# Performance work log

Measured on AMD Instinct MI355X. Metric: run time of the kernel, lower is better.

## Reference

```python
import jax, jax.numpy as jnp
import numpy as np

D_MODEL = 1024
B, T_Q, T_KV = 4, 2048, 2048


def _linear_params(key, d_in, d_out):
    kw, kb = jax.random.split(key)
    W = jax.random.normal(kw, (d_out, d_in), dtype=jnp.float32) * 0.02
    b = jax.random.normal(kb, (d_out,), dtype=jnp.float32) * 0.02
    return W, b


def setup_inputs() -> dict:
    key = jax.random.key(0)
    ks = jax.random.split(key, 7)
    latent_space = jax.random.normal(ks[0], (B, T_Q, D_MODEL), dtype=jnp.float32)
    input_space = jax.random.normal(ks[1], (B, T_KV, D_MODEL), dtype=jnp.float32)
    Wl, bl = _linear_params(ks[2], D_MODEL, D_MODEL)
    Wu, bu = _linear_params(ks[3], D_MODEL, D_MODEL)
    WA, bA = _linear_params(ks[4], D_MODEL, D_MODEL)  # A_proj: d -> J (J = d)
    WV, bV = _linear_params(ks[5], D_MODEL, D_MODEL)  # V_proj: J -> d
    Wo, bo = _linear_params(ks[6], D_MODEL, D_MODEL)
    return {
        "latent_space": latent_space, "input_space": input_space,
        "Wl": Wl, "bl": bl, "Wu": Wu, "bu": bu,
        "WA": WA, "bA": bA, "WV": WV, "bV": bV,
        "Wo": Wo, "bo": bo,
    }


def reference(latent_space, input_space, Wl, bl, Wu, bu, WA, bA, WV, bV, Wo, bo):
    # emb_0 = l_proj(latent)            [B, T_q, d]
    emb0 = jnp.einsum('bqd,ed->bqe', latent_space, Wl) + bl
    # l = softmax(u_proj(emb_0), -1)^T  [B, d, T_q]
    l = jax.nn.softmax(jnp.einsum('bqd,ed->bqe', emb0, Wu) + bu, axis=-1)
    l = jnp.swapaxes(l, -2, -1)
    # D = A_proj(input)                 [B, T_kv, J]
    Dm = jnp.einsum('bkd,jd->bkj', input_space, WA) + bA
    # A = softmax(V_proj(D), dim=-2)    softmax over T_kv
    A = jax.nn.softmax(jnp.einsum('bkj,dj->bkd', Dm, WV) + bV, axis=-2)
    # w = A @ l                         [B, T_kv, T_q]
    w = jnp.einsum('bkd,bdq->bkq', A, l)
    # o = w @ o_proj(latent)            [B, T_kv, d]
    ov = jnp.einsum('bqd,ed->bqe', latent_space, Wo) + bo
    o = jnp.einsum('bkq,bqd->bkd', w, ov)
    return o
```

## Files before the change

kernel.cpp:

```cpp
#include <hip/hip_runtime.h>
#include <hip/hip_bf16.h>
#include <stdint.h>

typedef __attribute__((ext_vector_type(8))) short bf16x8;
typedef __attribute__((ext_vector_type(4))) float f32x4;
typedef __attribute__((ext_vector_type(4))) unsigned short u16x4;

#define B_  4
#define T_  2048
#define D_  1024

__device__ __forceinline__ float bf2f(ushort u) {
  union { unsigned int i; float f; } v; v.i = ((unsigned int)u) << 16; return v.f;
}
__device__ __forceinline__ ushort f2bf(float f) {
  return (ushort)(__bfloat16_as_ushort(__float2bfloat16(f)));
}
__device__ __forceinline__ void async16(const void* g, void* l) {
  __builtin_amdgcn_global_load_lds(
      (const __attribute__((address_space(1))) void*)g,
      (__attribute__((address_space(3))) void*)l, 16, 0, 0);
}

__global__ __launch_bounds__(256)
void prep(const float* __restrict__ lat, const float* __restrict__ inp,
          const float* __restrict__ Wl, const float* __restrict__ bl,
          const float* __restrict__ Wu, const float* __restrict__ bu,
          const float* __restrict__ WA, const float* __restrict__ bA,
          const float* __restrict__ WV, const float* __restrict__ bV,
          const float* __restrict__ Wo, const float* __restrict__ bo,
          ushort* __restrict__ xBf, ushort* __restrict__ xBf2,
          ushort* __restrict__ w1, ushort* __restrict__ w2,
          ushort* __restrict__ wCatWo, float* __restrict__ bc, float* __restrict__ bc2)
{
  __shared__ alignas(16) ushort t[64 * 65];
  const long NW = (long)D_ * D_;
  const int bx = blockIdx.x;
  const int tid = threadIdx.x;
  if (bx < 16384) {
    const float* in = bx < 8192 ? lat : inp;
    ushort* out = bx < 8192 ? xBf : xBf2;
    const long i = (long)(bx & 8191) * 256 + tid;
    const float4 v = *(const float4*)(in + i * 4);
    u16x4 o;
    o[0] = f2bf(v.x); o[1] = f2bf(v.y); o[2] = f2bf(v.z); o[3] = f2bf(v.w);
    *(u16x4*)(out + i * 4) = o;
  } else if (bx < 19456) {
    const int seg = (bx - 16384) >> 10;
    const float* in  = seg == 0 ? Wu : (seg == 1 ? WV : Wo);
    ushort* out = seg == 0 ? w1 : (seg == 1 ? w1 + NW : wCatWo);
    const long i = (long)((bx - 16384) & 1023) * 256 + tid;
    const float4 v = *(const float4*)(in + i * 4);
    u16x4 o;
    o[0] = f2bf(v.x); o[1] = f2bf(v.y); o[2] = f2bf(v.z); o[3] = f2bf(v.w);
    *(u16x4*)(out + i * 4) = o;
  } else if (bx < 19968) {
    const int z = (bx - 19456) >> 8;
    const int w = (bx - 19456) & 255;
    const float* in = z ? WA : Wl;
    ushort* out = z ? w2 + NW : w2;
    const int c0 = (w & 15) * 64, r0 = (w >> 4) * 64;
    const int tx = tid & 15, ty = tid >> 4;
#pragma unroll
    for (int i = 0; i < 4; ++i) {
      const int r = ty + i * 16;
      const float4 v = *(const float4*)(in + (long)(r0 + r) * D_ + c0 + tx * 4);
      t[(tx * 4 + 0) * 65 + r] = f2bf(v.x);
      t[(tx * 4 + 1) * 65 + r] = f2bf(v.y);
      t[(tx * 4 + 2) * 65 + r] = f2bf(v.z);
      t[(tx * 4 + 3) * 65 + r] = f2bf(v.w);
    }
    __syncthreads();
#pragma unroll
    for (int i = 0; i < 4; ++i) {
      const int c = ty + i * 16;
      u16x4 v;
#pragma unroll
      for (int j = 0; j < 4; ++j) v[j] = t[c * 65 + tx * 4 + j];
      *(u16x4*)(out + (long)(c0 + c) * D_ + r0 + tx * 4) = v;
    }
  } else {
    const int z = (bx - 19968) >> 8;
    const int w = (bx - 19968) & 255;
    const float* W    = z ? WV : Wu;
    const float* bin  = z ? bA : bl;
    const float* badd = z ? bV : bu;
    float* out        = z ? bc2 : bc;
    const int wv = tid >> 6, lane = tid & 63;
    const int e = w * 4 + wv;
    const float* row = W + (long)e * D_;
    float s = 0.f;
#pragma unroll
    for (int i = 0; i < 16; ++i) s += row[lane + i * 64] * bin[lane + i * 64];
#pragma unroll
    for (int off = 32; off; off >>= 1) s += __shfl_xor(s, off);
    if (lane == 0) out[e] = s + badd[e];
  }
}

#define PH_SYNC_IN()                                               \
  __builtin_amdgcn_s_barrier();                                    \
  asm volatile("s_waitcnt lgkmcnt(0)" ::: "memory");               \
  __builtin_amdgcn_sched_barrier(0);                               \
  __builtin_amdgcn_s_setprio(1)
#define PH_SYNC_OUT()                                              \
  __builtin_amdgcn_s_setprio(0);                                   \
  __builtin_amdgcn_s_barrier()


__global__ __launch_bounds__(512, 2)
void gemm256(const ushort* __restrict__ A, const ushort* __restrict__ Bm,
             const float* __restrict__ bias1, const float* __restrict__ bias2,
             ushort* __restrict__ C1, ushort* __restrict__ C2,
             int ldA, int ldB)
{
  __shared__ alignas(16) ushort AbS[2 * 16384];
  __shared__ alignas(16) ushort BbS[3 * 16384];

  const int gx = gridDim.x;
  const int nwg = gx * gridDim.y;
  int fid = blockIdx.y * gx + blockIdx.x;
  fid = (fid & 7) * (nwg >> 3) + (fid >> 3);
  const int bx = fid % gx;
  const int by = fid / gx;
  const int tileM = by * 256, tileN = bx * 256;

  const int tid  = threadIdx.x;
  const int wid  = tid >> 6;
  const int lane = tid & 63;
  const int wm   = wid >> 2;
  const int wn   = wid & 3;

  const int srow8 = tid >> 3;
  const int scol8 = ((tid & 7) ^ (srow8 & 7)) << 3;
  const ushort* gAs = A  + (long)(tileM + srow8) * ldA + scol8;
  const ushort* gBs = Bm + (long)(tileN + srow8) * ldB + scol8;
  const int sdst = tid << 3;

#define STA(b, i, t) async16(gAs + (long)((i) * 64) * ldA + (t) * 64, \
                             AbS + (b) * 16384 + (i) * 4096 + sdst)
#define STB(b, i, t) async16(gBs + (long)((i) * 64) * ldB + (t) * 64, \
                             BbS + (b) * 16384 + (i) * 4096 + sdst)

  const int frow = lane & 15;
  const int kg   = lane >> 4;
  const int ck0 = ((kg       ^ (frow & 7)) << 3);
  const int ck1 = (((4 + kg) ^ (frow & 7)) << 3);
  int aoffr[8], boffr[4];
#pragma unroll
  for (int mi = 0; mi < 8; ++mi) aoffr[mi] = (wm * 128 + mi * 16 + frow) * 64;
#pragma unroll
  for (int n = 0; n < 4; ++n)    boffr[n]  = (wn * 64 + n * 16 + frow) * 64;

  f32x4 acc[8][4];
#pragma unroll
  for (int i = 0; i < 8; ++i)
#pragma unroll
    for (int j = 0; j < 4; ++j) acc[i][j] = (f32x4){0.f, 0.f, 0.f, 0.f};

#pragma unroll
  for (int i = 0; i < 4; ++i) STA(0, i, 0);
#pragma unroll
  for (int i = 0; i < 4; ++i) STB(0, i, 0);
#pragma unroll
  for (int i = 0; i < 4; ++i) STA(1, i, 1);
#pragma unroll
  for (int i = 0; i < 4; ++i) STB(1, i, 1);
  asm volatile("s_waitcnt vmcnt(8)" ::: "memory");
  __builtin_amdgcn_s_barrier();

#pragma unroll 1
  for (int t = 0; t < 16; ++t) {
    const int buf = t & 1;
    const int bB  = t - (t / 3) * 3;
    const int nA  = (t + 1) & 1;
    const int nB  = (t + 2) - ((t + 2) / 3) * 3;
    const ushort* Ac = AbS + buf * 16384;
    const ushort* Bc = BbS + bB * 16384;
    bf16x8 fa[4], fb[4], ga[4];

#pragma unroll
    for (int n = 0; n < 4; ++n) fb[n] = *(const bf16x8*)(Bc + boffr[n] + ck0);
#pragma unroll
    for (int m = 0; m < 4; ++m) fa[m] = *(const bf16x8*)(Ac + aoffr[m] + ck0);
    if (t >= 1 && t <= 14) { STA(nA, 0, t + 1); STA(nA, 1, t + 1); }
    PH_SYNC_IN();
#pragma unroll
    for (int m = 0; m < 4; ++m)
#pragma unroll
      for (int n = 0; n < 4; ++n)
        acc[m][n] = __builtin_amdgcn_mfma_f32_16x16x32_bf16(fa[m], fb[n], acc[m][n], 0, 0, 0);
    PH_SYNC_OUT();

#pragma unroll
    for (int m = 0; m < 4; ++m) ga[m] = *(const bf16x8*)(Ac + aoffr[4 + m] + ck0);
    if (t >= 1 && t <= 14) { STA(nA, 2, t + 1); STA(nA, 3, t + 1); }
    if (t <= 13)           { STB(nB, 0, t + 2); STB(nB, 1, t + 2); }
    PH_SYNC_IN();
#pragma unroll
    for (int m = 0; m < 4; ++m)
#pragma unroll
      for (int n = 0; n < 4; ++n)
        acc[4 + m][n] = __builtin_amdgcn_mfma_f32_16x16x32_bf16(ga[m], fb[n], acc[4 + m][n], 0, 0, 0);
    PH_SYNC_OUT();

#pragma unroll
    for (int n = 0; n < 4; ++n) fb[n] = *(const bf16x8*)(Bc + boffr[n] + ck1);
#pragma unroll
    for (int m = 0; m < 4; ++m) fa[m] = *(const bf16x8*)(Ac + aoffr[m] + ck1);
    if (t <= 13) { STB(nB, 2, t + 2); STB(nB, 3, t + 2); }
    PH_SYNC_IN();
#pragma unroll
    for (int m = 0; m < 4; ++m)
#pragma unroll
      for (int n = 0; n < 4; ++n)
        acc[m][n] = __builtin_amdgcn_mfma_f32_16x16x32_bf16(fa[m], fb[n], acc[m][n], 0, 0, 0);
    PH_SYNC_OUT();

#pragma unroll
    for (int m = 0; m < 4; ++m) ga[m] = *(const bf16x8*)(Ac + aoffr[4 + m] + ck1);
    if (t <= 13)      { asm volatile("s_waitcnt vmcnt(4)" ::: "memory"); }
    else if (t == 14) { asm volatile("s_waitcnt vmcnt(0)" ::: "memory"); }
    PH_SYNC_IN();
#pragma unroll
    for (int m = 0; m < 4; ++m)
#pragma unroll
      for (int n = 0; n < 4; ++n)
        acc[4 + m][n] = __builtin_amdgcn_mfma_f32_16x16x32_bf16(ga[m], fb[n], acc[4 + m][n], 0, 0, 0);
    PH_SYNC_OUT();
  }
#undef STA
#undef STB

  const bool second = tileN >= 1024;
  ushort* Cp = second ? C2 : C1;
  const float* bb = second ? bias2 : bias1;
  const int cb = tileN - (second ? 1024 : 0) + wn * 64 + (lane & 15);
  const int rb = tileM + wm * 128 + ((lane >> 4) << 2);
#pragma unroll
  for (int mi = 0; mi < 8; ++mi) {
    const int mrow = rb + mi * 16;
#pragma unroll
    for (int ni = 0; ni < 4; ++ni) {
      const int col = cb + ni * 16;
      const float bv = bb[col];
#pragma unroll
      for (int r = 0; r < 4; ++r)
        Cp[(long)(mrow + r) * 1024 + col] = f2bf(acc[mi][ni][r] + bv);
    }
  }
}

template<int MODE>
__global__ __launch_bounds__(512, 2)
void gemm128(const ushort* __restrict__ A, const ushort* __restrict__ Bm,
             const float* __restrict__ bias1, void* __restrict__ C1,
             int ldA, int ldB, long sAz, long sBz, long sCz)
{
  __shared__ alignas(16) ushort AbS[3 * 16384];
  __shared__ alignas(16) ushort BbS[3 * 8192];

  const int gx = gridDim.x, gy = gridDim.y;
  const int nwg = gx * gy * gridDim.z;
  int fid = (blockIdx.z * gy + blockIdx.y) * gx + blockIdx.x;
  fid = (fid & 7) * (nwg >> 3) + (fid >> 3);
  const int bx = fid % gx;
  const int by = (fid / gx) % gy;
  const int bz = fid / (gx * gy);
  const int tileM = by * 256, tileN = bx * 128;

  const ushort* Ap = A;
  const ushort* Bp = Bm;
  if constexpr (MODE == 2) {
    Ap += (long)(bz >> 1) * sAz + (long)(bz & 1) * 1024;
    Bp += (long)(bz >> 1) * sBz + (long)(bz & 1) * 1024;
  } else {
    Ap += (long)bz * sAz;
    Bp += (long)bz * sBz;
  }

  const int tid  = threadIdx.x;
  const int wid  = tid >> 6;
  const int lane = tid & 63;
  const int wm   = wid >> 1;
  const int wn   = wid & 1;

  const int srow8 = tid >> 3;
  const int scol8 = ((tid & 7) ^ (srow8 & 7)) << 3;
  const ushort* gAs = Ap + (long)(tileM + srow8) * ldA + scol8;
  const ushort* gBs = Bp + (long)(tileN + srow8) * ldB + scol8;
  const int sdst = tid << 3;

#define STA(b, i, t) async16(gAs + (long)((i) * 64) * ldA + (t) * 64, \
                             AbS + (b) * 16384 + (i) * 4096 + sdst)
#define STB(b, i, t) async16(gBs + (long)((i) * 64) * ldB + (t) * 64, \
                             BbS + (b) * 8192 + (i) * 4096 + sdst)

  const int frow = lane & 15;
  const int kg   = lane >> 4;
  const int ck0 = ((kg       ^ (frow & 7)) << 3);
  const int ck1 = (((4 + kg) ^ (frow & 7)) << 3);
  int aoffr[4], boffr[4];
#pragma unroll
  for (int mi = 0; mi < 4; ++mi) aoffr[mi] = (wm * 64 + mi * 16 + frow) * 64;
#pragma unroll
  for (int n = 0; n < 4; ++n)    boffr[n]  = (wn * 64 + n * 16 + frow) * 64;

  f32x4 acc[4][4];
#pragma unroll
  for (int i = 0; i < 4; ++i)
#pragma unroll
    for (int j = 0; j < 4; ++j) acc[i][j] = (f32x4){0.f, 0.f, 0.f, 0.f};

#pragma unroll
  for (int i = 0; i < 4; ++i) STA(0, i, 0);
  STB(0, 0, 0); STB(0, 1, 0);
#pragma unroll
  for (int i = 0; i < 4; ++i) STA(1, i, 1);
  STB(1, 0, 1); STB(1, 1, 1);
  asm volatile("s_waitcnt vmcnt(6)" ::: "memory");
  __builtin_amdgcn_s_barrier();

#pragma unroll 1
  for (int t = 0; t < 16; ++t) {
    const int bufT = t - (t / 3) * 3;
    const int nb   = (t + 2) - ((t + 2) / 3) * 3;
    const ushort* Ac = AbS + bufT * 16384;
    const ushort* Bc = BbS + bufT * 8192;
    bf16x8 fa[4], fb[4];

#pragma unroll
    for (int n = 0; n < 4; ++n) fb[n] = *(const bf16x8*)(Bc + boffr[n] + ck0);
#pragma unroll
    for (int m = 0; m < 4; ++m) fa[m] = *(const bf16x8*)(Ac + aoffr[m] + ck0);
    if (t <= 13) { STA(nb, 0, t + 2); STA(nb, 1, t + 2); STA(nb, 2, t + 2); STA(nb, 3, t + 2); }
    PH_SYNC_IN();
#pragma unroll
    for (int m = 0; m < 4; ++m)
#pragma unroll
      for (int n = 0; n < 4; ++n)
        acc[m][n] = __builtin_amdgcn_mfma_f32_16x16x32_bf16(fa[m], fb[n], acc[m][n], 0, 0, 0);
    PH_SYNC_OUT();

#pragma unroll
    for (int n = 0; n < 4; ++n) fb[n] = *(const bf16x8*)(Bc + boffr[n] + ck1);
#pragma unroll
    for (int m = 0; m < 4; ++m) fa[m] = *(const bf16x8*)(Ac + aoffr[m] + ck1);
    if (t <= 13) { STB(nb, 0, t + 2); STB(nb, 1, t + 2); }
    if (t <= 13)      { asm volatile("s_waitcnt vmcnt(6)" ::: "memory"); }
    else if (t == 14) { asm volatile("s_waitcnt vmcnt(0)" ::: "memory"); }
    PH_SYNC_IN();
#pragma unroll
    for (int m = 0; m < 4; ++m)
#pragma unroll
      for (int n = 0; n < 4; ++n)
        acc[m][n] = __builtin_amdgcn_mfma_f32_16x16x32_bf16(fa[m], fb[n], acc[m][n], 0, 0, 0);
    PH_SYNC_OUT();
  }
#undef STA
#undef STB

  const int cb = tileN + wn * 64 + (lane & 15);
  const int rb = tileM + wm * 64 + ((lane >> 4) << 2);

  if constexpr (MODE == 0) {
    ushort* Cp = (ushort*)C1 + (long)bz * sCz;
#pragma unroll
    for (int ni = 0; ni < 4; ++ni) {
      const int col = cb + ni * 16;
#pragma unroll
      for (int mi = 0; mi < 4; ++mi)
#pragma unroll
        for (int r = 0; r < 4; ++r)
          Cp[(long)(rb + mi * 16 + r) * 1024 + col] = f2bf(acc[mi][ni][r]);
    }
  } else if constexpr (MODE == 1) {
    ushort* Cp = (ushort*)C1;
#pragma unroll
    for (int ni = 0; ni < 4; ++ni) {
      const int col = cb + ni * 16;
      const float bv = bias1[col];
#pragma unroll
      for (int mi = 0; mi < 4; ++mi)
#pragma unroll
        for (int r = 0; r < 4; ++r)
          Cp[(long)(rb + mi * 16 + r) * 1024 + col] = f2bf(__expf(acc[mi][ni][r] + bv));
    }
  } else if constexpr (MODE == 2) {
    ushort* Cp = (ushort*)C1 + ((long)(bz & 1) * B_ + (bz >> 1)) * ((long)D_ * D_);
#pragma unroll
    for (int ni = 0; ni < 4; ++ni) {
      const int col = cb + ni * 16;
#pragma unroll
      for (int mi = 0; mi < 4; ++mi)
#pragma unroll
        for (int r = 0; r < 4; ++r)
          Cp[(long)(rb + mi * 16 + r) * 1024 + col] = f2bf(acc[mi][ni][r]);
    }
  } else {
    float* Cp = (float*)C1 + (long)bz * sCz;
#pragma unroll
    for (int ni = 0; ni < 4; ++ni) {
      const int col = cb + ni * 16;
#pragma unroll
      for (int mi = 0; mi < 4; ++mi)
#pragma unroll
        for (int r = 0; r < 4; ++r)
          Cp[(long)(rb + mi * 16 + r) * 1024 + col] = acc[mi][ni][r];
    }
  }
}

__global__ __launch_bounds__(256)
void reduce2_scale(const ushort* __restrict__ P, const float* __restrict__ cinv,
                   ushort* __restrict__ MT)
{
  const long stride = (long)B_ * D_ * D_;
  const long base = ((long)blockIdx.x * 256 + threadIdx.x) * 8;
  const int b = (int)(base >> 20);
  const int e0 = (int)(base & (D_ - 1));
  bf16x8 p0 = *(const bf16x8*)(P + base);
  bf16x8 p1 = *(const bf16x8*)(P + stride + base);
  const float4 c0 = *(const float4*)(cinv + (long)b * D_ + e0);
  const float4 c1 = *(const float4*)(cinv + (long)b * D_ + e0 + 4);
  const float cc[8] = {c0.x, c0.y, c0.z, c0.w, c1.x, c1.y, c1.z, c1.w};
  bf16x8 o;
#pragma unroll
  for (int j = 0; j < 8; ++j)
    o[j] = (short)f2bf((bf2f((ushort)p0[j]) + bf2f((ushort)p1[j])) * cc[j]);
  *(bf16x8*)(MT + base) = o;
}

__global__ __launch_bounds__(256)
void softmax_row(ushort* __restrict__ S)
{
  const long base = (long)blockIdx.x * D_;
  const int tid = threadIdx.x;
  float e[4], s = 0.f;
#pragma unroll
  for (int i = 0; i < 4; ++i) { e[i] = __expf(bf2f(S[base + i * 256 + tid])); s += e[i]; }
#pragma unroll
  for (int off = 32; off; off >>= 1) s += __shfl_xor(s, off);
  __shared__ float reds[4];
  if ((tid & 63) == 0) reds[tid >> 6] = s;
  __syncthreads();
  s = reds[0] + reds[1] + reds[2] + reds[3];
  const float inv = 1.f / s;
#pragma unroll
  for (int i = 0; i < 4; ++i)
    S[base + i * 256 + tid] = f2bf(e[i] * inv);
}

__global__ __launch_bounds__(256)
void transpose2(const ushort* __restrict__ l, ushort* __restrict__ lT,
                const ushort* __restrict__ ov, ushort* __restrict__ ovT)
{
  __shared__ alignas(16) ushort t[64 * 65];
  const int z = blockIdx.z;
  const int b = z & (B_ - 1);
  const ushort* in = (z < B_ ? l : ov) + (long)b * T_ * D_;
  ushort* out      = (z < B_ ? lT : ovT) + (long)b * (long)D_ * T_;
  const int c0 = blockIdx.x * 64, r0 = blockIdx.y * 64;
  const int tx = threadIdx.x & 15, ty = threadIdx.x >> 4;
#pragma unroll
  for (int i = 0; i < 4; ++i) {
    const int r = ty + i * 16;
    u16x4 v = *(const u16x4*)(in + (long)(r0 + r) * D_ + c0 + tx * 4);
#pragma unroll
    for (int c = 0; c < 4; ++c) t[(tx * 4 + c) * 65 + r] = v[c];
  }
  __syncthreads();
#pragma unroll
  for (int i = 0; i < 4; ++i) {
    const int c = ty + i * 16;
    u16x4 v;
#pragma unroll
    for (int j = 0; j < 4; ++j) v[j] = t[c * 65 + tx * 4 + j];
    *(u16x4*)(out + (long)(c0 + c) * T_ + r0 + tx * 4) = v;
  }
}

__global__ __launch_bounds__(256)
void colsum_part(const ushort* __restrict__ E, float* __restrict__ psum)
{
  const int d = blockIdx.x * 256 + threadIdx.x;
  const int c = blockIdx.y;
  const int b = blockIdx.z;
  const ushort* p = E + ((long)b * T_ + (long)c * 128) * D_ + d;
  float s = 0.f;
#pragma unroll 4
  for (int r = 0; r < 128; ++r) s += bf2f(p[(long)r * D_]);
  psum[((long)b * 16 + c) * D_ + d] = s;
}

__global__ __launch_bounds__(256)
void colsum_comb(const float* __restrict__ psum, float* __restrict__ cinv)
{
  const int d = blockIdx.x * 256 + threadIdx.x;
  const int b = blockIdx.y;
  float s = 0.f;
#pragma unroll
  for (int c = 0; c < 16; ++c) s += psum[((long)b * 16 + c) * D_ + d];
  cinv[(long)b * D_ + d] = 1.f / s;
}

extern "C" void kernel_launch(void* const* d_in, const int* in_sizes, int n_in,
                              void* d_out, int out_size, void* d_ws, size_t ws_size,
                              hipStream_t stream)
{
  (void)in_sizes; (void)n_in; (void)out_size; (void)ws_size;
  const float* lat = (const float*)d_in[0];
  const float* inp = (const float*)d_in[1];
  const float* Wl  = (const float*)d_in[2];
  const float* bl  = (const float*)d_in[3];
  const float* Wu  = (const float*)d_in[4];
  const float* bu  = (const float*)d_in[5];
  const float* WA  = (const float*)d_in[6];
  const float* bA  = (const float*)d_in[7];
  const float* WV  = (const float*)d_in[8];
  const float* bV  = (const float*)d_in[9];
  const float* Wo  = (const float*)d_in[10];
  const float* bo  = (const float*)d_in[11];

  char* w = (char*)d_ws;
  auto carve = [&](size_t bytes) { char* p = w; w += (bytes + 255) & ~(size_t)255; return p; };
  const long NT = (long)B_ * T_ * D_;
  const long NW = (long)D_ * D_;
  ushort* xBf   = (ushort*)carve(NT * 2);
  ushort* xBf2  = (ushort*)carve(NT * 2);
  ushort* bufA  = (ushort*)carve(NT * 2);
  ushort* bufB  = (ushort*)carve(NT * 2);
  ushort* scr   = (ushort*)carve(NT * 2);
  ushort* MT    = (ushort*)carve((long)B_ * NW * 2);
  ushort* wCat  = (ushort*)carve(3 * NW * 2);
  float*  bc    = (float*)carve(D_ * 4);
  float*  bc2   = (float*)carve(D_ * 4);
  float*  psum  = (float*)carve(64 * 1024 * 4);
  float*  cinv  = (float*)carve(8 * 1024 * 4);
  ushort* w1 = scr;
  ushort* w2 = scr + 2 * NW;
  ushort* ovT = scr;
  ushort* part = bufB;

  const dim3 blk(256, 1, 1);
  const dim3 blk5(512, 1, 1);

  prep<<<dim3(20480), blk, 0, stream>>>(lat, inp, Wl, bl, Wu, bu, WA, bA, WV, bV, Wo, bo,
                                        xBf, xBf2, w1, w2, wCat + NW, bc, bc2);
  gemm128<0><<<dim3(8, 4, 2), blk5, 0, stream>>>(
      w1, w2, nullptr, wCat, D_, D_, NW, NW, 2 * NW);
  gemm256<<<dim3(8, 32, 1), blk5, 0, stream>>>(
      xBf, wCat, bc, bo, bufB, bufA, D_, D_);
  softmax_row<<<dim3(B_ * T_), blk, 0, stream>>>(bufB);
  transpose2<<<dim3(16, 32, 2 * B_), blk, 0, stream>>>(bufB, xBf, bufA, ovT);
  gemm128<2><<<dim3(8, 4, 8), blk5, 0, stream>>>(
      ovT, xBf, nullptr, part, T_, T_, (long)D_ * T_, (long)D_ * T_, 0);
  gemm128<1><<<dim3(8, 32, 1), blk5, 0, stream>>>(
      xBf2, wCat + 2 * NW, bc2, bufA, D_, D_, 0, 0, 0);
  colsum_part<<<dim3(4, 16, B_), blk, 0, stream>>>(bufA, psum);
  colsum_comb<<<dim3(4, B_, 1), blk, 0, stream>>>(psum, cinv);
  reduce2_scale<<<dim3(2048), blk, 0, stream>>>(part, cinv, MT);
  gemm128<3><<<dim3(8, 8, 4), blk5, 0, stream>>>(
      bufA, MT, nullptr, d_out, D_, D_,
      (long)T_ * D_, NW, (long)T_ * D_);
}
```

Before: 309.6 us.

## Split-K weight product, fuse column sums into GEMM epilogue, fold softmax into transpose

The weight-product GEMM is now split-K four ways across 256 blocks, with a separate reduce kernel, to raise parallelism over the previous 64-block launch. The column-sum for the softmax over T_kv is folded into the exp GEMM epilogue as wave shuffles plus atomicAdd, with psum zeroed in prep, which removes the two colsum kernels. Row softmax is split into a read-only row-sum kernel, and the normalisation moves into the transpose, saving one write and one read of the full activation. Costs are atomic contention, an extra exp per element, split-K partials rounded to bf16 before summation, and a nondeterministic summation order.

New measurement: 292.0 us. 1.06x faster.

```diff
diff --git a/kernel.cpp b/kernel.cpp
--- a/kernel.cpp
+++ b/kernel.cpp
@@ -31,7 +31,8 @@
           const float* __restrict__ Wo, const float* __restrict__ bo,
           ushort* __restrict__ xBf, ushort* __restrict__ xBf2,
           ushort* __restrict__ w1, ushort* __restrict__ w2,
-          ushort* __restrict__ wCatWo, float* __restrict__ bc, float* __restrict__ bc2)
+          ushort* __restrict__ wCatWo, float* __restrict__ bc, float* __restrict__ bc2,
+          float* __restrict__ psum)
 {
   __shared__ alignas(16) ushort t[64 * 65];
   const long NW = (long)D_ * D_;
@@ -79,7 +80,7 @@
       for (int j = 0; j < 4; ++j) v[j] = t[c * 65 + tx * 4 + j];
       *(u16x4*)(out + (long)(c0 + c) * D_ + r0 + tx * 4) = v;
     }
-  } else {
+  } else if (bx < 20480) {
     const int z = (bx - 19968) >> 8;
     const int w = (bx - 19968) & 255;
     const float* W    = z ? WV : Wu;
@@ -95,6 +96,8 @@
 #pragma unroll
     for (int off = 32; off; off >>= 1) s += __shfl_xor(s, off);
     if (lane == 0) out[e] = s + badd[e];
+  } else {
+    psum[(bx - 20480) * 256 + tid] = 0.f;
   }
 }
 
@@ -106,7 +109,6 @@
 #define PH_SYNC_OUT()                                              \
   __builtin_amdgcn_s_setprio(0);                                   \
   __builtin_amdgcn_s_barrier()
-
 
 __global__ __launch_bounds__(512, 2)
 void gemm256(const ushort* __restrict__ A, const ushort* __restrict__ Bm,
@@ -251,11 +253,12 @@
   }
 }
 
-template<int MODE>
+template<int MODE, int NKT = 16>
 __global__ __launch_bounds__(512, 2)
 void gemm128(const ushort* __restrict__ A, const ushort* __restrict__ Bm,
              const float* __restrict__ bias1, void* __restrict__ C1,
-             int ldA, int ldB, long sAz, long sBz, long sCz)
+             int ldA, int ldB, long sAz, long sBz, long sCz,
+             float* __restrict__ psumG)
 {
   __shared__ alignas(16) ushort AbS[3 * 16384];
   __shared__ alignas(16) ushort BbS[3 * 8192];
@@ -274,6 +277,9 @@
   if constexpr (MODE == 2) {
     Ap += (long)(bz >> 1) * sAz + (long)(bz & 1) * 1024;
     Bp += (long)(bz >> 1) * sBz + (long)(bz & 1) * 1024;
+  } else if constexpr (MODE == 4) {
+    Ap += (long)(bz >> 2) * sAz + (long)(bz & 3) * 256;
+    Bp += (long)(bz >> 2) * sBz + (long)(bz & 3) * 256;
   } else {
     Ap += (long)bz * sAz;
     Bp += (long)bz * sBz;
@@ -322,7 +328,7 @@
   __builtin_amdgcn_s_barrier();
 
 #pragma unroll 1
-  for (int t = 0; t < 16; ++t) {
+  for (int t = 0; t < NKT; ++t) {
     const int bufT = t - (t / 3) * 3;
     const int nb   = (t + 2) - ((t + 2) / 3) * 3;
     const ushort* Ac = AbS + bufT * 16384;
@@ -333,7 +339,7 @@
     for (int n = 0; n < 4; ++n) fb[n] = *(const bf16x8*)(Bc + boffr[n] + ck0);
 #pragma unroll
     for (int m = 0; m < 4; ++m) fa[m] = *(const bf16x8*)(Ac + aoffr[m] + ck0);
-    if (t <= 13) { STA(nb, 0, t + 2); STA(nb, 1, t + 2); STA(nb, 2, t + 2); STA(nb, 3, t + 2); }
+    if (t <= NKT - 3) { STA(nb, 0, t + 2); STA(nb, 1, t + 2); STA(nb, 2, t + 2); STA(nb, 3, t + 2); }
     PH_SYNC_IN();
 #pragma unroll
     for (int m = 0; m < 4; ++m)
@@ -346,9 +352,9 @@
     for (int n = 0; n < 4; ++n) fb[n] = *(const bf16x8*)(Bc + boffr[n] + ck1);
 #pragma unroll
     for (int m = 0; m < 4; ++m) fa[m] = *(const bf16x8*)(Ac + aoffr[m] + ck1);
-    if (t <= 13) { STB(nb, 0, t + 2); STB(nb, 1, t + 2); }
-    if (t <= 13)      { asm volatile("s_waitcnt vmcnt(6)" ::: "memory"); }
-    else if (t == 14) { asm volatile("s_waitcnt vmcnt(0)" ::: "memory"); }
+    if (t <= NKT - 3) { STB(nb, 0, t + 2); STB(nb, 1, t + 2); }
+    if (t <= NKT - 3)      { asm volatile("s_waitcnt vmcnt(6)" ::: "memory"); }
+    else if (t == NKT - 2) { asm volatile("s_waitcnt vmcnt(0)" ::: "memory"); }
     PH_SYNC_IN();
 #pragma unroll
     for (int m = 0; m < 4; ++m)
@@ -363,28 +369,25 @@
   const int cb = tileN + wn * 64 + (lane & 15);
   const int rb = tileM + wm * 64 + ((lane >> 4) << 2);
 
-  if constexpr (MODE == 0) {
-    ushort* Cp = (ushort*)C1 + (long)bz * sCz;
-#pragma unroll
-    for (int ni = 0; ni < 4; ++ni) {
-      const int col = cb + ni * 16;
-#pragma unroll
-      for (int mi = 0; mi < 4; ++mi)
-#pragma unroll
-        for (int r = 0; r < 4; ++r)
-          Cp[(long)(rb + mi * 16 + r) * 1024 + col] = f2bf(acc[mi][ni][r]);
-    }
-  } else if constexpr (MODE == 1) {
+  if constexpr (MODE == 1) {
     ushort* Cp = (ushort*)C1;
+    const int bE = tileM >> 11;
 #pragma unroll
     for (int ni = 0; ni < 4; ++ni) {
       const int col = cb + ni * 16;
       const float bv = bias1[col];
+      float cs = 0.f;
 #pragma unroll
       for (int mi = 0; mi < 4; ++mi)
 #pragma unroll
-        for (int r = 0; r < 4; ++r)
-          Cp[(long)(rb + mi * 16 + r) * 1024 + col] = f2bf(__expf(acc[mi][ni][r] + bv));
+        for (int r = 0; r < 4; ++r) {
+          const ushort ev = f2bf(__expf(acc[mi][ni][r] + bv));
+          Cp[(long)(rb + mi * 16 + r) * 1024 + col] = ev;
+          cs += bf2f(ev);
+        }
+      cs += __shfl_xor(cs, 16);
+      cs += __shfl_xor(cs, 32);
+      if ((lane >> 4) == 0) atomicAdd(psumG + (long)bE * D_ + col, cs);
     }
   } else if constexpr (MODE == 2) {
     ushort* Cp = (ushort*)C1 + ((long)(bz & 1) * B_ + (bz >> 1)) * ((long)D_ * D_);
@@ -397,6 +400,18 @@
         for (int r = 0; r < 4; ++r)
           Cp[(long)(rb + mi * 16 + r) * 1024 + col] = f2bf(acc[mi][ni][r]);
     }
+  } else if constexpr (MODE == 4) {
+    const int comp = bz >> 2, sp = bz & 3;
+    ushort* Cp = (ushort*)C1 + ((long)sp * 2 + comp) * ((long)D_ * D_);
+#pragma unroll
+    for (int ni = 0; ni < 4; ++ni) {
+      const int col = cb + ni * 16;
+#pragma unroll
+      for (int mi = 0; mi < 4; ++mi)
+#pragma unroll
+        for (int r = 0; r < 4; ++r)
+          Cp[(long)(rb + mi * 16 + r) * 1024 + col] = f2bf(acc[mi][ni][r]);
+    }
   } else {
     float* Cp = (float*)C1 + (long)bz * sCz;
 #pragma unroll
@@ -412,7 +427,80 @@
 }
 
 __global__ __launch_bounds__(256)
-void reduce2_scale(const ushort* __restrict__ P, const float* __restrict__ cinv,
+void reduce4(const ushort* __restrict__ P, ushort* __restrict__ wCat)
+{
+  const long NW = (long)D_ * D_;
+  const long i = ((long)blockIdx.x * 256 + threadIdx.x) * 8;
+  float s[8] = {0.f, 0.f, 0.f, 0.f, 0.f, 0.f, 0.f, 0.f};
+#pragma unroll
+  for (int sp = 0; sp < 4; ++sp) {
+    bf16x8 p = *(const bf16x8*)(P + (long)sp * 2 * NW + i);
+#pragma unroll
+    for (int j = 0; j < 8; ++j) s[j] += bf2f((ushort)p[j]);
+  }
+  const long comp = (i >= NW) ? 1 : 0;
+  ushort* out = wCat + comp * 2 * NW + (i - comp * NW);
+  bf16x8 o;
+#pragma unroll
+  for (int j = 0; j < 8; ++j) o[j] = (short)f2bf(s[j]);
+  *(bf16x8*)out = o;
+}
+
+__global__ __launch_bounds__(256)
+void rowexp_inv(const ushort* __restrict__ S, float* __restrict__ rinv)
+{
+  const long base = (long)blockIdx.x * D_;
+  const int tid = threadIdx.x;
+  float s = 0.f;
+#pragma unroll
+  for (int i = 0; i < 4; ++i) s += __expf(bf2f(S[base + i * 256 + tid]));
+#pragma unroll
+  for (int off = 32; off; off >>= 1) s += __shfl_xor(s, off);
+  __shared__ float reds[4];
+  if ((tid & 63) == 0) reds[tid >> 6] = s;
+  __syncthreads();
+  if (tid == 0) rinv[blockIdx.x] = 1.f / (reds[0] + reds[1] + reds[2] + reds[3]);
+}
+
+__global__ __launch_bounds__(256)
+void transposeF(const ushort* __restrict__ l, ushort* __restrict__ lT,
+                const ushort* __restrict__ ov, ushort* __restrict__ ovT,
+                const float* __restrict__ rinv)
+{
+  __shared__ alignas(16) ushort t[64 * 65];
+  const int z = blockIdx.z;
+  const int b = z & (B_ - 1);
+  const bool isL = z < B_;
+  const ushort* in = (isL ? l : ov) + (long)b * T_ * D_;
+  ushort* out      = (isL ? lT : ovT) + (long)b * (long)D_ * T_;
+  const int c0 = blockIdx.x * 64, r0 = blockIdx.y * 64;
+  const int tx = threadIdx.x & 15, ty = threadIdx.x >> 4;
+#pragma unroll
+  for (int i = 0; i < 4; ++i) {
+    const int r = ty + i * 16;
+    u16x4 v = *(const u16x4*)(in + (long)(r0 + r) * D_ + c0 + tx * 4);
+    if (isL) {
+      const float ri = rinv[(long)b * T_ + r0 + r];
+#pragma unroll
+      for (int c = 0; c < 4; ++c) t[(tx * 4 + c) * 65 + r] = f2bf(__expf(bf2f(v[c])) * ri);
+    } else {
+#pragma unroll
+      for (int c = 0; c < 4; ++c) t[(tx * 4 + c) * 65 + r] = v[c];
+    }
+  }
+  __syncthreads();
+#pragma unroll
+  for (int i = 0; i < 4; ++i) {
+    const int c = ty + i * 16;
+    u16x4 v;
+#pragma unroll
+    for (int j = 0; j < 4; ++j) v[j] = t[c * 65 + tx * 4 + j];
+    *(u16x4*)(out + (long)(c0 + c) * T_ + r0 + tx * 4) = v;
+  }
+}
+
+__global__ __launch_bounds__(256)
+void reduce2_scale(const ushort* __restrict__ P, const float* __restrict__ psum,
                    ushort* __restrict__ MT)
 {
   const long stride = (long)B_ * D_ * D_;
@@ -421,87 +509,15 @@
   const int e0 = (int)(base & (D_ - 1));
   bf16x8 p0 = *(const bf16x8*)(P + base);
   bf16x8 p1 = *(const bf16x8*)(P + stride + base);
-  const float4 c0 = *(const float4*)(cinv + (long)b * D_ + e0);
-  const float4 c1 = *(const float4*)(cinv + (long)b * D_ + e0 + 4);
-  const float cc[8] = {c0.x, c0.y, c0.z, c0.w, c1.x, c1.y, c1.z, c1.w};
+  const float4 c0 = *(const float4*)(psum + (long)b * D_ + e0);
+  const float4 c1 = *(const float4*)(psum + (long)b * D_ + e0 + 4);
+  const float cc[8] = {1.f / c0.x, 1.f / c0.y, 1.f / c0.z, 1.f / c0.w,
+                       1.f / c1.x, 1.f / c1.y, 1.f / c1.z, 1.f / c1.w};
   bf16x8 o;
 #pragma unroll
   for (int j = 0; j < 8; ++j)
     o[j] = (short)f2bf((bf2f((ushort)p0[j]) + bf2f((ushort)p1[j])) * cc[j]);
   *(bf16x8*)(MT + base) = o;
-}
-
-__global__ __launch_bounds__(256)
-void softmax_row(ushort* __restrict__ S)
-{
-  const long base = (long)blockIdx.x * D_;
-  const int tid = threadIdx.x;
-  float e[4], s = 0.f;
-#pragma unroll
-  for (int i = 0; i < 4; ++i) { e[i] = __expf(bf2f(S[base + i * 256 + tid])); s += e[i]; }
-#pragma unroll
-  for (int off = 32; off; off >>= 1) s += __shfl_xor(s, off);
-  __shared__ float reds[4];
-  if ((tid & 63) == 0) reds[tid >> 6] = s;
-  __syncthreads();
-  s = reds[0] + reds[1] + reds[2] + reds[3];
-  const float inv = 1.f / s;
-#pragma unroll
-  for (int i = 0; i < 4; ++i)
-    S[base + i * 256 + tid] = f2bf(e[i] * inv);
-}
-
-__global__ __launch_bounds__(256)
-void transpose2(const ushort* __restrict__ l, ushort* __restrict__ lT,
-                const ushort* __restrict__ ov, ushort* __restrict__ ovT)
-{
-  __shared__ alignas(16) ushort t[64 * 65];
-  const int z = blockIdx.z;
-  const int b = z & (B_ - 1);
-  const ushort* in = (z < B_ ? l : ov) + (long)b * T_ * D_;
-  ushort* out      = (z < B_ ? lT : ovT) + (long)b * (long)D_ * T_;
-  const int c0 = blockIdx.x * 64, r0 = blockIdx.y * 64;
-  const int tx = threadIdx.x & 15, ty = threadIdx.x >> 4;
-#pragma unroll
-  for (int i = 0; i < 4; ++i) {
-    const int r = ty + i * 16;
-    u16x4 v = *(const u16x4*)(in + (long)(r0 + r) * D_ + c0 + tx * 4);
-#pragma unroll
-    for (int c = 0; c < 4; ++c) t[(tx * 4 + c) * 65 + r] = v[c];
-  }
-  __syncthreads();
-#pragma unroll
-  for (int i = 0; i < 4; ++i) {
-    const int c = ty + i * 16;
-    u16x4 v;
-#pragma unroll
-    for (int j = 0; j < 4; ++j) v[j] = t[c * 65 + tx * 4 + j];
-    *(u16x4*)(out + (long)(c0 + c) * T_ + r0 + tx * 4) = v;
-  }
-}
-
-__global__ __launch_bounds__(256)
-void colsum_part(const ushort* __restrict__ E, float* __restrict__ psum)
-{
-  const int d = blockIdx.x * 256 + threadIdx.x;
-  const int c = blockIdx.y;
-  const int b = blockIdx.z;
-  const ushort* p = E + ((long)b * T_ + (long)c * 128) * D_ + d;
-  float s = 0.f;
-#pragma unroll 4
-  for (int r = 0; r < 128; ++r) s += bf2f(p[(long)r * D_]);
-  psum[((long)b * 16 + c) * D_ + d] = s;
-}
-
-__global__ __launch_bounds__(256)
-void colsum_comb(const float* __restrict__ psum, float* __restrict__ cinv)
-{
-  const int d = blockIdx.x * 256 + threadIdx.x;
-  const int b = blockIdx.y;
-  float s = 0.f;
-#pragma unroll
-  for (int c = 0; c < 16; ++c) s += psum[((long)b * 16 + c) * D_ + d];
-  cinv[(long)b * D_ + d] = 1.f / s;
 }
 
 extern "C" void kernel_launch(void* const* d_in, const int* in_sizes, int n_in,
@@ -535,32 +551,32 @@
   ushort* wCat  = (ushort*)carve(3 * NW * 2);
   float*  bc    = (float*)carve(D_ * 4);
   float*  bc2   = (float*)carve(D_ * 4);
-  float*  psum  = (float*)carve(64 * 1024 * 4);
-  float*  cinv  = (float*)carve(8 * 1024 * 4);
+  float*  psum  = (float*)carve((long)B_ * D_ * 4);
+  float*  rinv  = (float*)carve((long)B_ * T_ * 4);
   ushort* w1 = scr;
   ushort* w2 = scr + 2 * NW;
+  ushort* Pc = bufA;
   ushort* ovT = scr;
   ushort* part = bufB;
 
   const dim3 blk(256, 1, 1);
   const dim3 blk5(512, 1, 1);
 
-  prep<<<dim3(20480), blk, 0, stream>>>(lat, inp, Wl, bl, Wu, bu, WA, bA, WV, bV, Wo, bo,
-                                        xBf, xBf2, w1, w2, wCat + NW, bc, bc2);
-  gemm128<0><<<dim3(8, 4, 2), blk5, 0, stream>>>(
-      w1, w2, nullptr, wCat, D_, D_, NW, NW, 2 * NW);
+  prep<<<dim3(20496), blk, 0, stream>>>(lat, inp, Wl, bl, Wu, bu, WA, bA, WV, bV, Wo, bo,
+                                        xBf, xBf2, w1, w2, wCat + NW, bc, bc2, psum);
+  gemm128<4, 4><<<dim3(8, 4, 8), blk5, 0, stream>>>(
+      w1, w2, nullptr, Pc, D_, D_, NW, NW, 0, nullptr);
+  reduce4<<<dim3(1024), blk, 0, stream>>>(Pc, wCat);
   gemm256<<<dim3(8, 32, 1), blk5, 0, stream>>>(
       xBf, wCat, bc, bo, bufB, bufA, D_, D_);
-  softmax_row<<<dim3(B_ * T_), blk, 0, stream>>>(bufB);
-  transpose2<<<dim3(16, 32, 2 * B_), blk, 0, stream>>>(bufB, xBf, bufA, ovT);
+  rowexp_inv<<<dim3(B_ * T_), blk, 0, stream>>>(bufB, rinv);
+  transposeF<<<dim3(16, 32, 2 * B_), blk, 0, stream>>>(bufB, xBf, bufA, ovT, rinv);
   gemm128<2><<<dim3(8, 4, 8), blk5, 0, stream>>>(
-      ovT, xBf, nullptr, part, T_, T_, (long)D_ * T_, (long)D_ * T_, 0);
+      ovT, xBf, nullptr, part, T_, T_, (long)D_ * T_, (long)D_ * T_, 0, nullptr);
   gemm128<1><<<dim3(8, 32, 1), blk5, 0, stream>>>(
-      xBf2, wCat + 2 * NW, bc2, bufA, D_, D_, 0, 0, 0);
-  colsum_part<<<dim3(4, 16, B_), blk, 0, stream>>>(bufA, psum);
-  colsum_comb<<<dim3(4, B_, 1), blk, 0, stream>>>(psum, cinv);
-  reduce2_scale<<<dim3(2048), blk, 0, stream>>>(part, cinv, MT);
+      xBf2, wCat + 2 * NW, bc2, bufA, D_, D_, 0, 0, 0, psum);
+  reduce2_scale<<<dim3(2048), blk, 0, stream>>>(part, psum, MT);
   gemm128<3><<<dim3(8, 8, 4), blk5, 0, stream>>>(
       bufA, MT, nullptr, d_out, D_, D_,
-      (long)T_ * D_, NW, (long)T_ * D_);
-}
+      (long)T_ * D_, NW, (long)T_ * D_, nullptr);
+}
```
